# Kernel tuning notes

Measured on AMD Instinct MI355X. Metric: run time of the kernel, lower is better.

The kernel has to match this reference:

```python
import jax, jax.numpy as jnp
import numpy as np
import math

HIDDEN = 2048
N_HEADS = 16
HEAD = HIDDEN // N_HEADS
B, S = 2, 2048


def setup_inputs() -> dict:
    key = jax.random.key(0)
    k1, k2, k3 = jax.random.split(key, 3)
    scale = 1.0 / math.sqrt(HIDDEN)
    return {
        "x": jax.random.normal(k1, (B, S, HIDDEN), dtype=jnp.float32),
        "w_qkv": jax.random.normal(k2, (HIDDEN, 3 * HIDDEN), dtype=jnp.float32) * scale,
        "b_qkv": jnp.zeros((3 * HIDDEN,), dtype=jnp.float32),
        "w_out": jax.random.normal(k3, (HIDDEN, HIDDEN), dtype=jnp.float32) * scale,
        "b_out": jnp.zeros((HIDDEN,), dtype=jnp.float32),
    }


def reference(x, w_qkv, b_qkv, w_out, b_out):
    b, s, _ = x.shape
    qkv = x @ w_qkv + b_qkv                      # [b, s, 3*hidden]
    q, k, v = jnp.split(qkv, 3, axis=-1)
    # 'b n (h l) -> b h n l'
    def heads(t):
        return t.reshape(b, s, N_HEADS, HEAD).transpose(0, 2, 1, 3)
    q, k, v = heads(q), heads(k), heads(v)
    scores = jnp.einsum("bhql,bhkl->bhqk", q, k) / math.sqrt(HEAD)
    # causal mask: positions where q_ind < k_ind get -10000 (matches source)
    q_ind = jnp.arange(s)[:, None]
    k_ind = jnp.arange(s)[None, :]
    scores = jnp.where(q_ind < k_ind, jnp.float32(-10000.0), scores)
    probs = jax.nn.softmax(scores, axis=-1)
    combined = jnp.einsum("bhqk,bhkl->bhql", probs, v)
    # 'b h q l -> b q (h l)'
    combined = combined.transpose(0, 2, 1, 3).reshape(b, s, HIDDEN)
    return combined @ w_out + b_out
```

## Files before the change

kernel.cpp:

```cpp
#include <hip/hip_runtime.h>
#include <hip/hip_bf16.h>

typedef __attribute__((ext_vector_type(4))) float f32x4;
typedef __attribute__((ext_vector_type(8))) short bf16x8;

#define GBL_AS(p) (const __attribute__((address_space(1))) void*)(p)
#define LDS_AS(p) (__attribute__((address_space(3))) void*)(p)

__device__ __forceinline__ void gload_lds16(const void* g, void* l) {
  __builtin_amdgcn_global_load_lds(GBL_AS(g), LDS_AS(l), 16, 0, 0);
}

__device__ __forceinline__ ushort f2bf(float f) {
  union { float f; unsigned int u; } v; v.f = f;
  unsigned int r = v.u + 0x7fffu + ((v.u >> 16) & 1u);
  return (ushort)(r >> 16);
}

__global__ void cast_f32_bf16_kernel(const float4* __restrict__ in,
                                     ushort4* __restrict__ out, int n4) {
  int i = blockIdx.x * 256 + threadIdx.x;
  if (i < n4) {
    float4 v = in[i];
    ushort4 o;
    o.x = f2bf(v.x); o.y = f2bf(v.y); o.z = f2bf(v.z); o.w = f2bf(v.w);
    out[i] = o;
  }
}

__global__ void transpose_cast_kernel(const float* __restrict__ in,
                                      ushort* __restrict__ out, int R, int C) {
  __shared__ float tile[64][65];
  int tx = threadIdx.x & 63, ty = threadIdx.x >> 6;
  int r0 = blockIdx.y * 64, c0 = blockIdx.x * 64;
#pragma unroll
  for (int i = 0; i < 64; i += 4)
    tile[ty + i][tx] = in[(size_t)(r0 + ty + i) * C + (c0 + tx)];
  __syncthreads();
#pragma unroll
  for (int i = 0; i < 64; i += 4)
    out[(size_t)(c0 + ty + i) * R + (r0 + tx)] = f2bf(tile[tx][ty + i]);
}

template <int MODE>
__global__ __launch_bounds__(256, 2) void gemm_bt_kernel(
    const ushort* __restrict__ A, const ushort* __restrict__ Bt,
    const float* __restrict__ bias, float* __restrict__ C,
    ushort* __restrict__ Qo, ushort* __restrict__ Ko, ushort* __restrict__ Vo,
    int M, int N, int K) {
  __shared__ ushort As[128 * 64];
  __shared__ ushort Bs[128 * 64];
  const int tid = threadIdx.x;
  const int w = tid >> 6, l = tid & 63;
  const int wr = w >> 1, wc = w & 1;
  const int m0 = blockIdx.y * 128, n0 = blockIdx.x * 128;

  f32x4 acc[4][4] = {};

  const int lr = l >> 3;
  const int lc = (l & 7) ^ lr;

  for (int k0 = 0; k0 < K; k0 += 64) {
#pragma unroll
    for (int i = 0; i < 4; ++i) {
      int row = i * 32 + w * 8 + lr;
      gload_lds16(A + (size_t)(m0 + row) * K + k0 + lc * 8,
                  (char*)As + (i * 32 + w * 8) * 128);
      gload_lds16(Bt + (size_t)(n0 + row) * K + k0 + lc * 8,
                  (char*)Bs + (i * 32 + w * 8) * 128);
    }
    __syncthreads();
    const char* Ab = (const char*)As;
    const char* Bb = (const char*)Bs;
#pragma unroll
    for (int ks = 0; ks < 2; ++ks) {
      bf16x8 af[4], bfr[4];
      int cc = ks * 4 + (l >> 4);
#pragma unroll
      for (int mi = 0; mi < 4; ++mi) {
        int row = wr * 64 + mi * 16 + (l & 15);
        af[mi] = *(const bf16x8*)(Ab + row * 128 + ((cc ^ (row & 7)) << 4));
      }
#pragma unroll
      for (int ni = 0; ni < 4; ++ni) {
        int row = wc * 64 + ni * 16 + (l & 15);
        bfr[ni] = *(const bf16x8*)(Bb + row * 128 + ((cc ^ (row & 7)) << 4));
      }
#pragma unroll
      for (int mi = 0; mi < 4; ++mi)
#pragma unroll
        for (int ni = 0; ni < 4; ++ni)
          acc[mi][ni] = __builtin_amdgcn_mfma_f32_16x16x32_bf16(
              af[mi], bfr[ni], acc[mi][ni], 0, 0, 0);
    }
    __syncthreads();
  }

  if (MODE == 0) {
#pragma unroll
    for (int mi = 0; mi < 4; ++mi) {
      int row = m0 + wr * 64 + mi * 16 + ((l >> 4) << 2);
#pragma unroll
      for (int ni = 0; ni < 4; ++ni) {
        int col = n0 + wc * 64 + ni * 16 + (l & 15);
        float b = bias[col];
#pragma unroll
        for (int r = 0; r < 4; ++r)
          C[(size_t)(row + r) * N + col] = acc[mi][ni][r] + b;
      }
    }
  } else {
    const float qscale = 0.08838834764831845f;
#pragma unroll
    for (int ni = 0; ni < 4; ++ni) {
      int n = n0 + wc * 64 + ni * 16 + (l & 15);
      int which = n >> 11;
      int cc2 = n & 2047;
      int h = cc2 >> 7, d = cc2 & 127;
      float b = bias[n];
#pragma unroll
      for (int mi = 0; mi < 4; ++mi) {
        int m = m0 + wr * 64 + mi * 16 + ((l >> 4) << 2);
        int bb = m >> 11, s = m & 2047;
        int bh = bb * 16 + h;
        if (which == 0) {
#pragma unroll
          for (int r = 0; r < 4; ++r)
            Qo[((size_t)bh * 2048 + s + r) * 128 + d] =
                f2bf((acc[mi][ni][r] + b) * qscale);
        } else if (which == 1) {
#pragma unroll
          for (int r = 0; r < 4; ++r)
            Ko[((size_t)bh * 2048 + s + r) * 128 + d] = f2bf(acc[mi][ni][r] + b);
        } else {
          ushort4 pk;
          pk.x = f2bf(acc[mi][ni][0] + b);
          pk.y = f2bf(acc[mi][ni][1] + b);
          pk.z = f2bf(acc[mi][ni][2] + b);
          pk.w = f2bf(acc[mi][ni][3] + b);
          *(ushort4*)(Vo + ((size_t)bh * 128 + d) * 2048 + s) = pk;
        }
      }
    }
  }
}

__global__ __launch_bounds__(512, 2) void attn_kernel(
    const ushort* __restrict__ Qg, const ushort* __restrict__ Kg,
    const ushort* __restrict__ Vtg, ushort* __restrict__ Og) {
  constexpr int S = 2048, D = 128;
  __shared__ ushort Kl[2][64 * 128];
  __shared__ ushort Vl[2][128 * 64];
  __shared__ ushort Pl[8][32 * 64];

  const int tid = threadIdx.x, w = tid >> 6, l = tid & 63;
  const int lid = blockIdx.x;
  const int bh = lid & 31;
  const int j = lid >> 5;
  const int g = w >> 2, wv = w & 3;
  const int qb = (g == 0) ? (8 + j) : (7 - j);
  const int wq0 = qb * 128 + wv * 32;
  const int nt_blk = 18 + 2 * j;

  const ushort* Qb = Qg + (size_t)bh * S * D;
  const ushort* Kb = Kg + (size_t)bh * S * D;
  const ushort* Vb = Vtg + (size_t)bh * D * S;

  bf16x8 qf[2][4];
#pragma unroll
  for (int rg = 0; rg < 2; ++rg)
#pragma unroll
    for (int ks = 0; ks < 4; ++ks)
      qf[rg][ks] = *(const bf16x8*)(Qb + (size_t)(wq0 + rg * 16 + (l & 15)) * D +
                                    ks * 32 + (l >> 4) * 8);

  f32x4 o[2][8] = {};
  float mrun[8], lrun[8], esc[8];
#pragma unroll
  for (int i = 0; i < 8; ++i) { mrun[i] = -1e30f; lrun[i] = 0.f; }

  auto stage = [&](int t, int buf) {
    const int k0 = t * 64;
#pragma unroll
    for (int s2 = 0; s2 < 2; ++s2) {
      int i = w * 2 + s2;
      int row = i * 4 + (l >> 4);
      int ck = (l & 15) ^ (row & 7);
      gload_lds16(Kb + (size_t)(k0 + row) * D + ck * 8,
                  (char*)Kl[buf] + i * 1024);
    }
#pragma unroll
    for (int s2 = 0; s2 < 2; ++s2) {
      int i = w * 2 + s2;
      int row = i * 8 + (l >> 3);
      int ck = (l & 7) ^ (row & 7);
      gload_lds16(Vb + (size_t)row * S + k0 + ck * 8,
                  (char*)Vl[buf] + i * 1024);
    }
  };

  stage(0, 0);

  for (int t = 0; t < nt_blk; ++t) {
    const int cur = t & 1;
    const int k0 = t * 64;
    if (t + 1 < nt_blk) {
      stage(t + 1, cur ^ 1);
      asm volatile("s_waitcnt vmcnt(4)" ::: "memory");
    } else {
      asm volatile("s_waitcnt vmcnt(0)" ::: "memory");
    }
    __builtin_amdgcn_s_barrier();

    const bool active = k0 < wq0 + 32;
    if (active) {
      const char* Kc = (const char*)Kl[cur];
      const char* Vc = (const char*)Vl[cur];
      f32x4 sa[2][4] = {};
#pragma unroll
      for (int ks = 0; ks < 4; ++ks) {
        bf16x8 kf[4];
        int cc = ks * 4 + (l >> 4);
#pragma unroll
        for (int cf = 0; cf < 4; ++cf) {
          int row = cf * 16 + (l & 15);
          kf[cf] = *(const bf16x8*)(Kc + row * 256 + ((cc ^ (row & 7)) << 4));
        }
        __builtin_amdgcn_s_setprio(1);
#pragma unroll
        for (int rg = 0; rg < 2; ++rg)
#pragma unroll
          for (int cf = 0; cf < 4; ++cf)
            sa[rg][cf] = __builtin_amdgcn_mfma_f32_16x16x32_bf16(
                qf[rg][ks], kf[cf], sa[rg][cf], 0, 0, 0);
        __builtin_amdgcn_s_setprio(0);
      }

      if (k0 + 63 > wq0) {
#pragma unroll
        for (int rg = 0; rg < 2; ++rg)
#pragma unroll
          for (int cf = 0; cf < 4; ++cf) {
            int kk = k0 + cf * 16 + (l & 15);
            int qrow = wq0 + rg * 16 + ((l >> 4) << 2);
#pragma unroll
            for (int r = 0; r < 4; ++r)
              if (qrow + r < kk) sa[rg][cf][r] = -1e9f;
          }
      }

#pragma unroll
      for (int rg = 0; rg < 2; ++rg) {
        float tmax[4] = {-1e30f, -1e30f, -1e30f, -1e30f};
#pragma unroll
        for (int cf = 0; cf < 4; ++cf)
#pragma unroll
          for (int r = 0; r < 4; ++r)
            tmax[r] = fmaxf(tmax[r], sa[rg][cf][r]);
#pragma unroll
        for (int r = 0; r < 4; ++r) {
          tmax[r] = fmaxf(tmax[r], __shfl_xor(tmax[r], 1));
          tmax[r] = fmaxf(tmax[r], __shfl_xor(tmax[r], 2));
          tmax[r] = fmaxf(tmax[r], __shfl_xor(tmax[r], 4));
          tmax[r] = fmaxf(tmax[r], __shfl_xor(tmax[r], 8));
        }
        float rsum[4] = {0.f, 0.f, 0.f, 0.f};
#pragma unroll
        for (int r = 0; r < 4; ++r) {
          int idx = rg * 4 + r;
          float mnew = fmaxf(mrun[idx], tmax[r]);
          esc[idx] = __expf(mrun[idx] - mnew);
          mrun[idx] = mnew;
        }
#pragma unroll
        for (int cf = 0; cf < 4; ++cf)
#pragma unroll
          for (int r = 0; r < 4; ++r) {
            float p = __expf(sa[rg][cf][r] - mrun[rg * 4 + r]);
            sa[rg][cf][r] = p;
            rsum[r] += p;
          }
#pragma unroll
        for (int r = 0; r < 4; ++r) {
          rsum[r] += __shfl_xor(rsum[r], 1);
          rsum[r] += __shfl_xor(rsum[r], 2);
          rsum[r] += __shfl_xor(rsum[r], 4);
          rsum[r] += __shfl_xor(rsum[r], 8);
          int idx = rg * 4 + r;
          lrun[idx] = lrun[idx] * esc[idx] + rsum[r];
        }
      }
#pragma unroll
      for (int rg = 0; rg < 2; ++rg)
#pragma unroll
        for (int df = 0; df < 8; ++df)
#pragma unroll
          for (int r = 0; r < 4; ++r)
            o[rg][df][r] *= esc[rg * 4 + r];

      char* Pb = (char*)Pl[w];
#pragma unroll
      for (int rg = 0; rg < 2; ++rg)
#pragma unroll
        for (int cf = 0; cf < 4; ++cf) {
          int col = cf * 16 + (l & 15);
          int cchunk = col >> 3, cin = col & 7;
#pragma unroll
          for (int r = 0; r < 4; ++r) {
            int row = rg * 16 + ((l >> 4) << 2) + r;
            *(ushort*)(Pb + row * 128 + ((cchunk ^ (row & 7)) << 4) + cin * 2) =
                f2bf(sa[rg][cf][r]);
          }
        }

#pragma unroll
      for (int ks = 0; ks < 2; ++ks) {
        bf16x8 pf[2];
        int cc = ks * 4 + (l >> 4);
#pragma unroll
        for (int rg = 0; rg < 2; ++rg) {
          int row = rg * 16 + (l & 15);
          pf[rg] = *(const bf16x8*)(Pb + row * 128 + ((cc ^ (row & 7)) << 4));
        }
        bf16x8 vf[8];
#pragma unroll
        for (int df = 0; df < 8; ++df) {
          int row = df * 16 + (l & 15);
          vf[df] = *(const bf16x8*)(Vc + row * 128 + ((cc ^ (row & 7)) << 4));
        }
        __builtin_amdgcn_s_setprio(1);
#pragma unroll
        for (int df = 0; df < 8; ++df)
#pragma unroll
          for (int rg = 0; rg < 2; ++rg)
            o[rg][df] = __builtin_amdgcn_mfma_f32_16x16x32_bf16(
                pf[rg], vf[df], o[rg][df], 0, 0, 0);
        __builtin_amdgcn_s_setprio(0);
      }
    }
    asm volatile("s_waitcnt lgkmcnt(0)" ::: "memory");
    __builtin_amdgcn_s_barrier();
  }

  const int b = bh >> 4, h = bh & 15;
#pragma unroll
  for (int rg = 0; rg < 2; ++rg)
#pragma unroll
    for (int r = 0; r < 4; ++r) {
      int idx = rg * 4 + r;
      float inv = 1.0f / lrun[idx];
      int s = wq0 + rg * 16 + ((l >> 4) << 2) + r;
#pragma unroll
      for (int df = 0; df < 8; ++df) {
        int col = h * 128 + df * 16 + (l & 15);
        Og[((size_t)b * 2048 + s) * 2048 + col] = f2bf(o[rg][df][r] * inv);
      }
    }
}

extern "C" void kernel_launch(void* const* d_in, const int* in_sizes, int n_in,
                              void* d_out, int out_size, void* d_ws,
                              size_t ws_size, hipStream_t stream) {
  const float* x = (const float*)d_in[0];
  const float* w_qkv = (const float*)d_in[1];
  const float* b_qkv = (const float*)d_in[2];
  const float* w_out = (const float*)d_in[3];
  const float* b_out = (const float*)d_in[4];
  float* out = (float*)d_out;
  char* ws = (char*)d_ws;

  if (ws_size < 92274688u) return;
  ushort* xb = (ushort*)(ws);
  ushort* wqkvt = (ushort*)(ws + 16777216);
  ushort* Q = (ushort*)(ws + 41943040);
  ushort* Kb = (ushort*)(ws + 58720256);
  ushort* Vt = (ushort*)(ws + 75497472);
  ushort* comb = xb;
  ushort* woutt = wqkvt;

  cast_f32_bf16_kernel<<<8192, 256, 0, stream>>>((const float4*)x, (ushort4*)xb,
                                                 2097152);
  transpose_cast_kernel<<<dim3(96, 32), 256, 0, stream>>>(w_qkv, wqkvt, 2048,
                                                          6144);
  gemm_bt_kernel<1><<<dim3(48, 32), 256, 0, stream>>>(
      xb, wqkvt, b_qkv, nullptr, Q, Kb, Vt, 4096, 6144, 2048);
  transpose_cast_kernel<<<dim3(32, 32), 256, 0, stream>>>(w_out, woutt, 2048,
                                                          2048);
  attn_kernel<<<dim3(256), 512, 0, stream>>>(Q, Kb, Vt, comb);
  gemm_bt_kernel<0><<<dim3(16, 32), 256, 0, stream>>>(
      comb, woutt, b_out, out, nullptr, nullptr, nullptr, 4096, 2048, 2048);
}
```

Before: 261.9 us.

## Use transposed 32x32x16 MFMA in attention to keep P in registers

The attention kernel switches from 16x16x32 MFMA to 32x32x16 MFMA and computes the transposed score tile (K·Qᵀ), so each lane owns a single query row. Softmax row reductions shrink to one cross-half shuffle, and the probability tile is repacked in registers with v_cvt_pk_bf16_f32 and permlane32_swap instead of a round trip through the LDS P buffer. Output stores become packed 8-byte writes. This removes LDS traffic and shuffle work but relies on a precise register-layout mapping and gfx950-specific instructions.

After: 233.7 us. -10.8%, faster.

```diff
diff --git a/kernel.cpp b/kernel.cpp
--- a/kernel.cpp
+++ b/kernel.cpp
@@ -2,6 +2,7 @@
 #include <hip/hip_bf16.h>
 
 typedef __attribute__((ext_vector_type(4))) float f32x4;
+typedef __attribute__((ext_vector_type(16))) float f32x16;
 typedef __attribute__((ext_vector_type(8))) short bf16x8;
 
 #define GBL_AS(p) (const __attribute__((address_space(1))) void*)(p)
@@ -151,7 +152,6 @@
   constexpr int S = 2048, D = 128;
   __shared__ ushort Kl[2][64 * 128];
   __shared__ ushort Vl[2][128 * 64];
-  __shared__ ushort Pl[8][32 * 64];
 
   const int tid = threadIdx.x, w = tid >> 6, l = tid & 63;
   const int lid = blockIdx.x;
@@ -161,23 +161,21 @@
   const int qb = (g == 0) ? (8 + j) : (7 - j);
   const int wq0 = qb * 128 + wv * 32;
   const int nt_blk = 18 + 2 * j;
+  const int ql = l & 31, h32 = l >> 5;
 
   const ushort* Qb = Qg + (size_t)bh * S * D;
   const ushort* Kb = Kg + (size_t)bh * S * D;
   const ushort* Vb = Vtg + (size_t)bh * D * S;
 
-  bf16x8 qf[2][4];
-#pragma unroll
-  for (int rg = 0; rg < 2; ++rg)
-#pragma unroll
-    for (int ks = 0; ks < 4; ++ks)
-      qf[rg][ks] = *(const bf16x8*)(Qb + (size_t)(wq0 + rg * 16 + (l & 15)) * D +
-                                    ks * 32 + (l >> 4) * 8);
-
-  f32x4 o[2][8] = {};
-  float mrun[8], lrun[8], esc[8];
-#pragma unroll
-  for (int i = 0; i < 8; ++i) { mrun[i] = -1e30f; lrun[i] = 0.f; }
+  bf16x8 qf[8];
+#pragma unroll
+  for (int ks = 0; ks < 8; ++ks)
+    qf[ks] = *(const bf16x8*)(Qb + (size_t)(wq0 + ql) * D + ks * 16 + h32 * 8);
+
+  f32x16 o[4];
+#pragma unroll
+  for (int dt = 0; dt < 4; ++dt) o[dt] = 0.f;
+  float mrun = -1e30f, lrun = 0.f;
 
   auto stage = [&](int t, int buf) {
     const int k0 = t * 64;
@@ -212,130 +210,95 @@
     }
     __builtin_amdgcn_s_barrier();
 
-    const bool active = k0 < wq0 + 32;
-    if (active) {
+    if (k0 < wq0 + 32) {
       const char* Kc = (const char*)Kl[cur];
       const char* Vc = (const char*)Vl[cur];
-      f32x4 sa[2][4] = {};
-#pragma unroll
-      for (int ks = 0; ks < 4; ++ks) {
-        bf16x8 kf[4];
-        int cc = ks * 4 + (l >> 4);
-#pragma unroll
-        for (int cf = 0; cf < 4; ++cf) {
-          int row = cf * 16 + (l & 15);
-          kf[cf] = *(const bf16x8*)(Kc + row * 256 + ((cc ^ (row & 7)) << 4));
-        }
-        __builtin_amdgcn_s_setprio(1);
-#pragma unroll
-        for (int rg = 0; rg < 2; ++rg)
-#pragma unroll
-          for (int cf = 0; cf < 4; ++cf)
-            sa[rg][cf] = __builtin_amdgcn_mfma_f32_16x16x32_bf16(
-                qf[rg][ks], kf[cf], sa[rg][cf], 0, 0, 0);
-        __builtin_amdgcn_s_setprio(0);
-      }
+
+      f32x16 sa[2];
+#pragma unroll
+      for (int kt = 0; kt < 2; ++kt) sa[kt] = 0.f;
+      __builtin_amdgcn_s_setprio(1);
+#pragma unroll
+      for (int kt = 0; kt < 2; ++kt) {
+        int row = kt * 32 + ql;
+        int swz = row & 7;
+#pragma unroll
+        for (int ks = 0; ks < 8; ++ks) {
+          int c = 2 * ks + h32;
+          bf16x8 kf = *(const bf16x8*)(Kc + row * 256 + ((c ^ swz) << 4));
+          sa[kt] = __builtin_amdgcn_mfma_f32_32x32x16_bf16(kf, qf[ks], sa[kt],
+                                                           0, 0, 0);
+        }
+      }
+      __builtin_amdgcn_s_setprio(0);
 
       if (k0 + 63 > wq0) {
-#pragma unroll
-        for (int rg = 0; rg < 2; ++rg)
-#pragma unroll
-          for (int cf = 0; cf < 4; ++cf) {
-            int kk = k0 + cf * 16 + (l & 15);
-            int qrow = wq0 + rg * 16 + ((l >> 4) << 2);
-#pragma unroll
-            for (int r = 0; r < 4; ++r)
-              if (qrow + r < kk) sa[rg][cf][r] = -1e9f;
+        int q = wq0 + ql;
+#pragma unroll
+        for (int kt = 0; kt < 2; ++kt) {
+          int kb = k0 + kt * 32 + 4 * h32;
+#pragma unroll
+          for (int r = 0; r < 16; ++r) {
+            int kk = kb + (r & 3) + 8 * (r >> 2);
+            if (q < kk) sa[kt][r] = -1e9f;
           }
-      }
-
-#pragma unroll
-      for (int rg = 0; rg < 2; ++rg) {
-        float tmax[4] = {-1e30f, -1e30f, -1e30f, -1e30f};
-#pragma unroll
-        for (int cf = 0; cf < 4; ++cf)
-#pragma unroll
-          for (int r = 0; r < 4; ++r)
-            tmax[r] = fmaxf(tmax[r], sa[rg][cf][r]);
-#pragma unroll
-        for (int r = 0; r < 4; ++r) {
-          tmax[r] = fmaxf(tmax[r], __shfl_xor(tmax[r], 1));
-          tmax[r] = fmaxf(tmax[r], __shfl_xor(tmax[r], 2));
-          tmax[r] = fmaxf(tmax[r], __shfl_xor(tmax[r], 4));
-          tmax[r] = fmaxf(tmax[r], __shfl_xor(tmax[r], 8));
-        }
-        float rsum[4] = {0.f, 0.f, 0.f, 0.f};
-#pragma unroll
-        for (int r = 0; r < 4; ++r) {
-          int idx = rg * 4 + r;
-          float mnew = fmaxf(mrun[idx], tmax[r]);
-          esc[idx] = __expf(mrun[idx] - mnew);
-          mrun[idx] = mnew;
-        }
-#pragma unroll
-        for (int cf = 0; cf < 4; ++cf)
-#pragma unroll
-          for (int r = 0; r < 4; ++r) {
-            float p = __expf(sa[rg][cf][r] - mrun[rg * 4 + r]);
-            sa[rg][cf][r] = p;
-            rsum[r] += p;
+        }
+      }
+
+      float tmax = -1e30f;
+#pragma unroll
+      for (int kt = 0; kt < 2; ++kt)
+#pragma unroll
+        for (int r = 0; r < 16; ++r) tmax = fmaxf(tmax, sa[kt][r]);
+      tmax = fmaxf(tmax, __shfl_xor(tmax, 32));
+      float mnew = fmaxf(mrun, tmax);
+      float e = __expf(mrun - mnew);
+      float rsum = 0.f;
+#pragma unroll
+      for (int kt = 0; kt < 2; ++kt)
+#pragma unroll
+        for (int r = 0; r < 16; ++r) {
+          float p = __expf(sa[kt][r] - mnew);
+          sa[kt][r] = p;
+          rsum += p;
+        }
+      rsum += __shfl_xor(rsum, 32);
+      lrun = lrun * e + rsum;
+      mrun = mnew;
+#pragma unroll
+      for (int dt = 0; dt < 4; ++dt) o[dt] *= e;
+
+#pragma unroll
+      for (int kt = 0; kt < 2; ++kt) {
+#pragma unroll
+        for (int u = 0; u < 2; ++u) {
+          int A0, B0, A1, B1;
+          asm("v_cvt_pk_bf16_f32 %0, %1, %2"
+              : "=v"(A0) : "v"(sa[kt][u * 8 + 0]), "v"(sa[kt][u * 8 + 1]));
+          asm("v_cvt_pk_bf16_f32 %0, %1, %2"
+              : "=v"(B0) : "v"(sa[kt][u * 8 + 2]), "v"(sa[kt][u * 8 + 3]));
+          asm("v_cvt_pk_bf16_f32 %0, %1, %2"
+              : "=v"(A1) : "v"(sa[kt][u * 8 + 4]), "v"(sa[kt][u * 8 + 5]));
+          asm("v_cvt_pk_bf16_f32 %0, %1, %2"
+              : "=v"(B1) : "v"(sa[kt][u * 8 + 6]), "v"(sa[kt][u * 8 + 7]));
+          auto r02 = __builtin_amdgcn_permlane32_swap(A0, A1, false, false);
+          auto r13 = __builtin_amdgcn_permlane32_swap(B0, B1, false, false);
+          union { int i[4]; bf16x8 v; } pu;
+          pu.i[0] = r02[0];
+          pu.i[1] = r13[0];
+          pu.i[2] = r02[1];
+          pu.i[3] = r13[1];
+          int c = 4 * kt + 2 * u + h32;
+          __builtin_amdgcn_s_setprio(1);
+#pragma unroll
+          for (int dt = 0; dt < 4; ++dt) {
+            int row = dt * 32 + ql;
+            bf16x8 vf = *(const bf16x8*)(Vc + row * 128 + ((c ^ (row & 7)) << 4));
+            o[dt] = __builtin_amdgcn_mfma_f32_32x32x16_bf16(vf, pu.v, o[dt],
+                                                            0, 0, 0);
           }
-#pragma unroll
-        for (int r = 0; r < 4; ++r) {
-          rsum[r] += __shfl_xor(rsum[r], 1);
-          rsum[r] += __shfl_xor(rsum[r], 2);
-          rsum[r] += __shfl_xor(rsum[r], 4);
-          rsum[r] += __shfl_xor(rsum[r], 8);
-          int idx = rg * 4 + r;
-          lrun[idx] = lrun[idx] * esc[idx] + rsum[r];
-        }
-      }
-#pragma unroll
-      for (int rg = 0; rg < 2; ++rg)
-#pragma unroll
-        for (int df = 0; df < 8; ++df)
-#pragma unroll
-          for (int r = 0; r < 4; ++r)
-            o[rg][df][r] *= esc[rg * 4 + r];
-
-      char* Pb = (char*)Pl[w];
-#pragma unroll
-      for (int rg = 0; rg < 2; ++rg)
-#pragma unroll
-        for (int cf = 0; cf < 4; ++cf) {
-          int col = cf * 16 + (l & 15);
-          int cchunk = col >> 3, cin = col & 7;
-#pragma unroll
-          for (int r = 0; r < 4; ++r) {
-            int row = rg * 16 + ((l >> 4) << 2) + r;
-            *(ushort*)(Pb + row * 128 + ((cchunk ^ (row & 7)) << 4) + cin * 2) =
-                f2bf(sa[rg][cf][r]);
-          }
-        }
-
-#pragma unroll
-      for (int ks = 0; ks < 2; ++ks) {
-        bf16x8 pf[2];
-        int cc = ks * 4 + (l >> 4);
-#pragma unroll
-        for (int rg = 0; rg < 2; ++rg) {
-          int row = rg * 16 + (l & 15);
-          pf[rg] = *(const bf16x8*)(Pb + row * 128 + ((cc ^ (row & 7)) << 4));
-        }
-        bf16x8 vf[8];
-#pragma unroll
-        for (int df = 0; df < 8; ++df) {
-          int row = df * 16 + (l & 15);
-          vf[df] = *(const bf16x8*)(Vc + row * 128 + ((cc ^ (row & 7)) << 4));
-        }
-        __builtin_amdgcn_s_setprio(1);
-#pragma unroll
-        for (int df = 0; df < 8; ++df)
-#pragma unroll
-          for (int rg = 0; rg < 2; ++rg)
-            o[rg][df] = __builtin_amdgcn_mfma_f32_16x16x32_bf16(
-                pf[rg], vf[df], o[rg][df], 0, 0, 0);
-        __builtin_amdgcn_s_setprio(0);
+          __builtin_amdgcn_s_setprio(0);
+        }
       }
     }
     asm volatile("s_waitcnt lgkmcnt(0)" ::: "memory");
@@ -343,18 +306,19 @@
   }
 
   const int b = bh >> 4, h = bh & 15;
-#pragma unroll
-  for (int rg = 0; rg < 2; ++rg)
-#pragma unroll
-    for (int r = 0; r < 4; ++r) {
-      int idx = rg * 4 + r;
-      float inv = 1.0f / lrun[idx];
-      int s = wq0 + rg * 16 + ((l >> 4) << 2) + r;
-#pragma unroll
-      for (int df = 0; df < 8; ++df) {
-        int col = h * 128 + df * 16 + (l & 15);
-        Og[((size_t)b * 2048 + s) * 2048 + col] = f2bf(o[rg][df][r] * inv);
-      }
+  float inv = 1.0f / lrun;
+  size_t rowbase = ((size_t)b * 2048 + (wq0 + ql)) * 2048 + h * 128;
+#pragma unroll
+  for (int dt = 0; dt < 4; ++dt)
+#pragma unroll
+    for (int r4 = 0; r4 < 4; ++r4) {
+      int col = dt * 32 + r4 * 8 + h32 * 4;
+      ushort4 pk;
+      pk.x = f2bf(o[dt][r4 * 4 + 0] * inv);
+      pk.y = f2bf(o[dt][r4 * 4 + 1] * inv);
+      pk.z = f2bf(o[dt][r4 * 4 + 2] * inv);
+      pk.w = f2bf(o[dt][r4 * 4 + 3] * inv);
+      *(ushort4*)(Og + rowbase + col) = pk;
     }
 }
 
```
